# Kernel optimization log

Hardware: AMD Instinct MI355X
Metric: run time of the kernel (lower is better)

## Reference

```python
import jax, jax.numpy as jnp
import numpy as np

B, S, D, H = 2, 2048, 1024, 16
DK = D // H  # 64

def setup_inputs() -> dict:
    key = jax.random.key(0)
    ks = jax.random.split(key, 8)
    xavier = np.sqrt(6.0 / (D + D))  # xavier_uniform bound for square Linear
    def lin_w(k):
        return jax.random.uniform(k, (D, D), jnp.float32, -xavier, xavier)
    return {
        'Q': jax.random.normal(ks[0], (B, S, D), jnp.float32),
        'length': jax.random.randint(ks[1], (B,), 1, S + 1, jnp.int32),
        'Wq': lin_w(ks[2]), 'bq': jnp.zeros((D,), jnp.float32),
        'Wk': lin_w(ks[3]), 'bk': jnp.zeros((D,), jnp.float32),
        'Wv': lin_w(ks[4]), 'bv': jnp.zeros((D,), jnp.float32),
    }

def reference(Q, length, Wq, bq, Wk, bk, Wv, bv):
    # project and split heads: [B,S,D] -> [B,H,S,DK]
    def heads(x, W, b):
        y = jnp.einsum('bsd,de->bse', x, W) + b
        return y.reshape(B, S, H, DK).transpose(0, 2, 1, 3)
    q = heads(Q, Wq, bq)
    k = heads(Q, Wk, bk)
    v = heads(Q, Wv, bv)
    scores = jnp.einsum('bhqd,bhkd->bhqk', q, k) / np.sqrt(DK)
    scores = jnp.exp(scores)  # NOTE: raw exp, no max-subtraction (faithful)
    # multiplicative key mask: mask[b,k] = k < length[b], broadcast over q,h
    mask = (jnp.arange(S)[None, :] < length[:, None]).astype(scores.dtype)
    scores = scores * mask[:, None, None, :]
    attn = scores / (jnp.sum(scores, axis=-1, keepdims=True) + 1e-8)
    ctx = jnp.einsum('bhqk,bhkd->bhqd', attn, v)
    return ctx.transpose(0, 2, 1, 3).reshape(B, S, D)
```

## Files before the change

kernel.cpp:

```cpp
#include <hip/hip_runtime.h>
#include <hip/hip_bf16.h>

#define B_  2
#define S_  2048
#define D_  1024
#define H_  16
#define DK_ 64
#define M_  (B_ * S_)

typedef short short8 __attribute__((ext_vector_type(8)));
typedef float float4v __attribute__((ext_vector_type(4)));

#define QSCALE 0.18033688011112042f

static __device__ __forceinline__ ushort f32_to_bf16bits(float f) {
    union { __hip_bfloat16 h; ushort u; } cv;
    cv.h = __float2bfloat16(f);
    return cv.u;
}

static __device__ __forceinline__ void glds16(const ushort* g, ushort* l) {
    __builtin_amdgcn_global_load_lds(
        (const __attribute__((address_space(1))) unsigned int*)g,
        (__attribute__((address_space(3))) unsigned int*)l, 16, 0, 0);
}

__global__ __launch_bounds__(256) void prep(
    const float* __restrict__ X, const float* __restrict__ W0,
    const float* __restrict__ W1, const float* __restrict__ W2,
    ushort* __restrict__ Xb, ushort* __restrict__ Wt)
{
    const int z = blockIdx.z;
    const int t = threadIdx.x;

    if (z >= 3) {
        const int blk = (z - 3) * 256 + blockIdx.y * 16 + blockIdx.x;
        const int i = blk * 2048 + t * 8;
        float4v a = *(const float4v*)(X + i);
        float4v b = *(const float4v*)(X + i + 4);
        short8 o;
        o[0] = (short)f32_to_bf16bits(a[0]); o[1] = (short)f32_to_bf16bits(a[1]);
        o[2] = (short)f32_to_bf16bits(a[2]); o[3] = (short)f32_to_bf16bits(a[3]);
        o[4] = (short)f32_to_bf16bits(b[0]); o[5] = (short)f32_to_bf16bits(b[1]);
        o[6] = (short)f32_to_bf16bits(b[2]); o[7] = (short)f32_to_bf16bits(b[3]);
        *(short8*)(Xb + i) = o;
        return;
    }

    const float* W = (z == 0) ? W0 : ((z == 1) ? W1 : W2);
    ushort* out = Wt + (size_t)z * D_ * D_;

    __shared__ ushort tile[64 * 72];
    int n0 = blockIdx.x * 64, k0 = blockIdx.y * 64;
    int r = t >> 3, g = t & 7;

    #pragma unroll
    for (int p = 0; p < 2; ++p) {
        int rr = r + p * 32;
        const float* src = W + (size_t)(k0 + rr) * D_ + n0 + g * 8;
        float4v a = *(const float4v*)src;
        float4v b = *(const float4v*)(src + 4);
        short8 o;
        o[0] = (short)f32_to_bf16bits(a[0]); o[1] = (short)f32_to_bf16bits(a[1]);
        o[2] = (short)f32_to_bf16bits(a[2]); o[3] = (short)f32_to_bf16bits(a[3]);
        o[4] = (short)f32_to_bf16bits(b[0]); o[5] = (short)f32_to_bf16bits(b[1]);
        o[6] = (short)f32_to_bf16bits(b[2]); o[7] = (short)f32_to_bf16bits(b[3]);
        *(short8*)&tile[rr * 72 + g * 8] = o;
    }
    __syncthreads();
    #pragma unroll
    for (int p = 0; p < 2; ++p) {
        int rr = r + p * 32;
        short8 v;
        #pragma unroll
        for (int i = 0; i < 8; ++i)
            v[i] = (short)tile[(g * 8 + i) * 72 + rr];
        *(short8*)(out + (size_t)(n0 + rr) * D_ + k0 + g * 8) = v;
    }
}

__global__ __launch_bounds__(256, 2) void proj_gemm(
    const ushort* __restrict__ X,
    const ushort* __restrict__ Wt,
    const float* __restrict__ b0, const float* __restrict__ b1,
    const float* __restrict__ b2,
    const int* __restrict__ length,
    ushort* __restrict__ qkv)
{
    const int m0 = blockIdx.x * 64, n0 = blockIdx.y * 128;
    const int bidx = m0 >> 11;
    const int s0 = m0 & (S_ - 1);
    const bool kv = (s0 < length[bidx]);

    __shared__ __align__(16) ushort As[64 * 64];
    __shared__ __align__(16) ushort Bs[3][128 * 64];

    const int t = threadIdx.x;
    const int lane = t & 63, wid = t >> 6;
    const int quad = lane >> 4, l16 = lane & 15;
    const int wr = wid >> 1, wc = wid & 1;

    float4v accq[2][4] = {}, acck[2][4] = {}, accv[2][4] = {};

    for (int kt = 0; kt < 16; ++kt) {
        const int k0 = kt * 64;
        __syncthreads();
        #pragma unroll
        for (int j = 0; j < 2; ++j) {
            const int cid = wid * 128 + j * 64 + lane;
            const int row = cid >> 3;
            const int cl  = (cid & 7) ^ (row & 7);
            glds16(X + (size_t)(m0 + row) * D_ + k0 + cl * 8, &As[cid * 8]);
        }
        #pragma unroll
        for (int j = 0; j < 4; ++j) {
            const int cid = wid * 256 + j * 64 + lane;
            const int row = cid >> 3;
            const int cl  = (cid & 7) ^ (row & 7);
            const size_t off = (size_t)(n0 + row) * D_ + k0 + cl * 8;
            glds16(Wt + off, &Bs[0][cid * 8]);
            if (kv) {
                glds16(Wt + (size_t)D_ * D_ + off,     &Bs[1][cid * 8]);
                glds16(Wt + (size_t)2 * D_ * D_ + off, &Bs[2][cid * 8]);
            }
        }
        __syncthreads();

        #pragma unroll
        for (int ks = 0; ks < 2; ++ks) {
            short8 a[2];
            #pragma unroll
            for (int i = 0; i < 2; ++i) {
                const int r = wr * 32 + i * 16 + l16;
                const int ph = (ks * 4 + quad) ^ (r & 7);
                a[i] = *(short8*)&As[r * 64 + ph * 8];
            }
            short8 bq[4];
            #pragma unroll
            for (int j = 0; j < 4; ++j) {
                const int r = wc * 64 + j * 16 + l16;
                const int ph = (ks * 4 + quad) ^ (r & 7);
                bq[j] = *(short8*)&Bs[0][r * 64 + ph * 8];
            }
            #pragma unroll
            for (int i = 0; i < 2; ++i)
                #pragma unroll
                for (int j = 0; j < 4; ++j)
                    accq[i][j] = __builtin_amdgcn_mfma_f32_16x16x32_bf16(
                        a[i], bq[j], accq[i][j], 0, 0, 0);
            if (kv) {
                short8 bk[4], bv[4];
                #pragma unroll
                for (int j = 0; j < 4; ++j) {
                    const int r = wc * 64 + j * 16 + l16;
                    const int ph = (ks * 4 + quad) ^ (r & 7);
                    bk[j] = *(short8*)&Bs[1][r * 64 + ph * 8];
                    bv[j] = *(short8*)&Bs[2][r * 64 + ph * 8];
                }
                #pragma unroll
                for (int i = 0; i < 2; ++i)
                    #pragma unroll
                    for (int j = 0; j < 4; ++j) {
                        acck[i][j] = __builtin_amdgcn_mfma_f32_16x16x32_bf16(
                            a[i], bk[j], acck[i][j], 0, 0, 0);
                        accv[i][j] = __builtin_amdgcn_mfma_f32_16x16x32_bf16(
                            a[i], bv[j], accv[i][j], 0, 0, 0);
                    }
            }
        }
    }

    #pragma unroll
    for (int j = 0; j < 4; ++j) {
        const int col = n0 + wc * 64 + j * 16 + l16;
        const int h = col >> 6, dk = col & (DK_ - 1);
        const float bvq = b0[col], bvk = b1[col], bvv = b2[col];
        #pragma unroll
        for (int i = 0; i < 2; ++i) {
            #pragma unroll
            for (int rr = 0; rr < 4; ++rr) {
                const int row = m0 + wr * 32 + i * 16 + quad * 4 + rr;
                const int s = row & (S_ - 1);
                const size_t hdr = ((size_t)(bidx * H_ + h) * S_ + s) * DK_ + dk;
                qkv[hdr] = f32_to_bf16bits((accq[i][j][rr] + bvq) * QSCALE);
                if (kv) {
                    qkv[(size_t)M_ * D_ + hdr] =
                        f32_to_bf16bits(acck[i][j][rr] + bvk);
                    qkv[(size_t)2 * M_ * D_ +
                        ((size_t)(bidx * H_ + h) * DK_ + dk) * S_ + s] =
                        f32_to_bf16bits(accv[i][j][rr] + bvv);
                }
            }
        }
    }
}

__global__ __launch_bounds__(256, 3) void attention(
    const ushort* __restrict__ qkv, const int* __restrict__ length,
    float* __restrict__ out)
{
    const int bid  = blockIdx.x;
    const int work = (bid & 7) * 128 + (bid >> 3);
    const int q0 = (work & 31) * 64;
    const int bh = work >> 5;
    const int b  = bh & 1;
    const int h  = bh >> 1;

    int len = length[b];
    if (len > S_) len = S_;
    if (len < 1) len = 1;
    const int nkt = (len + 63) >> 6;

    const ushort* qb = qkv + ((size_t)(b * H_ + h) * S_ + q0) * DK_;
    const ushort* kb = qkv + (size_t)M_ * D_ + (size_t)(b * H_ + h) * S_ * DK_;
    const ushort* vb = qkv + (size_t)2 * M_ * D_ + (size_t)(b * H_ + h) * DK_ * S_;

    __shared__ __align__(16) ushort Ks[3][64 * 64];
    __shared__ __align__(16) ushort Vs[3][64 * 64];

    const int t = threadIdx.x, lane = t & 63, wid = t >> 6;
    const int quad = lane >> 4, l16 = lane & 15;

    const int klocal = ((l16 >> 2) << 3) + (l16 & 3);
    const int hk     = (l16 & 3) | (((l16 >> 2) & 1) << 2);

    short8 qfrag[2];
    {
        const ushort* qp = qb + (size_t)(wid * 16 + l16) * DK_;
        qfrag[0] = *(const short8*)(qp + quad * 8);
        qfrag[1] = *(const short8*)(qp + (4 + quad) * 8);
    }

    auto stageKV = [&](int buf, int tile) {
        #pragma unroll
        for (int j = 0; j < 2; ++j) {
            const int cid = wid * 128 + j * 64 + lane;
            const int row = cid >> 3;
            const int c   = cid & 7;
            const int hKr = (row & 3) | (((row >> 3) & 1) << 2);
            glds16(kb + (size_t)(tile * 64 + row) * DK_ + (c ^ hKr) * 8,
                   &Ks[buf][cid * 8]);
            glds16(vb + (size_t)row * S_ + tile * 64 + (c ^ (row & 7)) * 8,
                   &Vs[buf][cid * 8]);
        }
    };

    stageKV(0, 0);
    if (nkt > 1) stageKV(1, 1);

    short8 ones8;
    #pragma unroll
    for (int i = 0; i < 8; ++i) ones8[i] = (short)0x3F80;

    float4v cacc[4] = {};
    float4v racc = {};

    int cur = 0;
    for (int kt = 0; kt < nkt; ++kt) {
        if (kt == nkt - 1) {
            asm volatile("s_waitcnt vmcnt(0) lgkmcnt(0)" ::: "memory");
        } else {
            asm volatile("s_waitcnt vmcnt(4) lgkmcnt(0)" ::: "memory");
        }
        __builtin_amdgcn_sched_barrier(0);
        __builtin_amdgcn_s_barrier();
        __builtin_amdgcn_sched_barrier(0);

        if (kt + 2 < nkt) {
            int sb = cur + 2; if (sb >= 3) sb -= 3;
            stageKV(sb, kt + 2);
        }

        float4v sacc[4] = {};
        #pragma unroll
        for (int ks = 0; ks < 2; ++ks) {
            #pragma unroll
            for (int ct = 0; ct < 4; ++ct) {
                const int krow = ((ct >> 1) << 5) + ((ct & 1) << 2) + klocal;
                const int pha = (ks * 4 + quad) ^ hk;
                short8 ak = *(short8*)&Ks[cur][krow * 64 + pha * 8];
                sacc[ct] = __builtin_amdgcn_mfma_f32_16x16x32_bf16(
                    ak, qfrag[ks], sacc[ct], 0, 0, 0);
            }
        }

        const bool full = ((kt + 1) * 64 <= len);
        short8 ap[2];
        #pragma unroll
        for (int ks = 0; ks < 2; ++ks) {
            union { uint u[4]; short8 s; } cv;
            #pragma unroll
            for (int hh = 0; hh < 2; ++hh) {
                const int ct = 2 * ks + hh;
                float e0 = __builtin_amdgcn_exp2f(sacc[ct][0]);
                float e1 = __builtin_amdgcn_exp2f(sacc[ct][1]);
                float e2 = __builtin_amdgcn_exp2f(sacc[ct][2]);
                float e3 = __builtin_amdgcn_exp2f(sacc[ct][3]);
                if (!full) {
                    const int kb0 = kt * 64 + ks * 32 + quad * 8 + hh * 4;
                    e0 = (kb0 + 0 < len) ? e0 : 0.f;
                    e1 = (kb0 + 1 < len) ? e1 : 0.f;
                    e2 = (kb0 + 2 < len) ? e2 : 0.f;
                    e3 = (kb0 + 3 < len) ? e3 : 0.f;
                }
                cv.u[hh * 2 + 0] = (__float_as_uint(e0) >> 16) |
                                   (__float_as_uint(e1) & 0xFFFF0000u);
                cv.u[hh * 2 + 1] = (__float_as_uint(e2) >> 16) |
                                   (__float_as_uint(e3) & 0xFFFF0000u);
            }
            ap[ks] = cv.s;
        }

        #pragma unroll
        for (int ks = 0; ks < 2; ++ks) {
            #pragma unroll
            for (int ct = 0; ct < 4; ++ct) {
                const int vrow = ct * 16 + l16;
                const int phv = (ks * 4 + quad) ^ (vrow & 7);
                short8 vv = *(short8*)&Vs[cur][vrow * 64 + phv * 8];
                cacc[ct] = __builtin_amdgcn_mfma_f32_16x16x32_bf16(
                    ap[ks], vv, cacc[ct], 0, 0, 0);
            }
            racc = __builtin_amdgcn_mfma_f32_16x16x32_bf16(
                ap[ks], ones8, racc, 0, 0, 0);
        }

        cur = cur + 1; if (cur == 3) cur = 0;
    }

    #pragma unroll
    for (int rr = 0; rr < 4; ++rr) {
        const float inv = 1.0f / (racc[rr] + 1e-8f);
        const int q = q0 + wid * 16 + quad * 4 + rr;
        #pragma unroll
        for (int ct = 0; ct < 4; ++ct) {
            const int d = h * 64 + ct * 16 + l16;
            out[((size_t)b * S_ + q) * D_ + d] = cacc[ct][rr] * inv;
        }
    }
}

extern "C" void kernel_launch(void* const* d_in, const int* in_sizes, int n_in,
                              void* d_out, int out_size, void* d_ws, size_t ws_size,
                              hipStream_t stream)
{
    const float* Q   = (const float*)d_in[0];
    const int*   len = (const int*)d_in[1];
    const float* Wq  = (const float*)d_in[2];
    const float* bq  = (const float*)d_in[3];
    const float* Wk  = (const float*)d_in[4];
    const float* bk  = (const float*)d_in[5];
    const float* Wv  = (const float*)d_in[6];
    const float* bv  = (const float*)d_in[7];
    float* out = (float*)d_out;

    ushort* ws  = (ushort*)d_ws;
    ushort* Xb  = ws;
    ushort* Wt  = ws + (size_t)M_ * D_;
    ushort* qkv = Wt + (size_t)3 * D_ * D_;

    dim3 gPr(16, 16, 11);
    prep<<<gPr, 256, 0, stream>>>(Q, Wq, Wk, Wv, Xb, Wt);

    dim3 gP(M_ / 64, D_ / 128);
    proj_gemm<<<gP, 256, 0, stream>>>(Xb, Wt, bq, bk, bv, len, qkv);

    attention<<<dim3(S_ / 64 * H_ * B_), 256, 0, stream>>>(qkv, len, out);
}
```

Before: 152.3 us.

## Process 128 queries per attention block to reuse staged K/V tiles

Each attention workgroup now covers 128 query rows instead of 64, so every wave runs two 16-row query tiles against each K/V tile staged in LDS. This halves the number of workgroups and the total K/V global-to-LDS traffic, and reuses each LDS fragment read across two MFMA chains. The block-to-work mapping is rewritten to match, and launch bounds drop from 3 to 2 blocks per CU to allow the larger accumulator register footprint. In exchange there are fewer blocks (512) to cover the GPU and lower occupancy.

```diff
diff --git a/kernel.cpp b/kernel.cpp
--- a/kernel.cpp
+++ b/kernel.cpp
@@ -195,16 +195,16 @@
     }
 }
 
-__global__ __launch_bounds__(256, 3) void attention(
+__global__ __launch_bounds__(256, 2) void attention(
     const ushort* __restrict__ qkv, const int* __restrict__ length,
     float* __restrict__ out)
 {
     const int bid  = blockIdx.x;
-    const int work = (bid & 7) * 128 + (bid >> 3);
-    const int q0 = (work & 31) * 64;
-    const int bh = work >> 5;
-    const int b  = bh & 1;
-    const int h  = bh >> 1;
+    const int work = (bid & 7) * 64 + (bid >> 3);
+    const int q0   = (work & 15) * 128;
+    const int hlo  = (work >> 4) & 1;
+    const int b    = (work >> 5) & 1;
+    const int h    = ((work >> 6) << 1) | hlo;
 
     int len = length[b];
     if (len > S_) len = S_;
@@ -224,11 +224,12 @@
     const int klocal = ((l16 >> 2) << 3) + (l16 & 3);
     const int hk     = (l16 & 3) | (((l16 >> 2) & 1) << 2);
 
-    short8 qfrag[2];
-    {
-        const ushort* qp = qb + (size_t)(wid * 16 + l16) * DK_;
-        qfrag[0] = *(const short8*)(qp + quad * 8);
-        qfrag[1] = *(const short8*)(qp + (4 + quad) * 8);
+    short8 qfrag[2][2];
+    #pragma unroll
+    for (int qt = 0; qt < 2; ++qt) {
+        const ushort* qp = qb + (size_t)(wid * 32 + qt * 16 + l16) * DK_;
+        qfrag[qt][0] = *(const short8*)(qp + quad * 8);
+        qfrag[qt][1] = *(const short8*)(qp + (4 + quad) * 8);
     }
 
     auto stageKV = [&](int buf, int tile) {
@@ -252,8 +253,8 @@
     #pragma unroll
     for (int i = 0; i < 8; ++i) ones8[i] = (short)0x3F80;
 
-    float4v cacc[4] = {};
-    float4v racc = {};
+    float4v cacc[2][4] = {};
+    float4v racc[2] = {};
 
     int cur = 0;
     for (int kt = 0; kt < nkt; ++kt) {
@@ -271,7 +272,7 @@
             stageKV(sb, kt + 2);
         }
 
-        float4v sacc[4] = {};
+        float4v sacc[2][4] = {};
         #pragma unroll
         for (int ks = 0; ks < 2; ++ks) {
             #pragma unroll
@@ -279,36 +280,41 @@
                 const int krow = ((ct >> 1) << 5) + ((ct & 1) << 2) + klocal;
                 const int pha = (ks * 4 + quad) ^ hk;
                 short8 ak = *(short8*)&Ks[cur][krow * 64 + pha * 8];
-                sacc[ct] = __builtin_amdgcn_mfma_f32_16x16x32_bf16(
-                    ak, qfrag[ks], sacc[ct], 0, 0, 0);
+                sacc[0][ct] = __builtin_amdgcn_mfma_f32_16x16x32_bf16(
+                    ak, qfrag[0][ks], sacc[0][ct], 0, 0, 0);
+                sacc[1][ct] = __builtin_amdgcn_mfma_f32_16x16x32_bf16(
+                    ak, qfrag[1][ks], sacc[1][ct], 0, 0, 0);
             }
         }
 
         const bool full = ((kt + 1) * 64 <= len);
-        short8 ap[2];
-        #pragma unroll
-        for (int ks = 0; ks < 2; ++ks) {
-            union { uint u[4]; short8 s; } cv;
-            #pragma unroll
-            for (int hh = 0; hh < 2; ++hh) {
-                const int ct = 2 * ks + hh;
-                float e0 = __builtin_amdgcn_exp2f(sacc[ct][0]);
-                float e1 = __builtin_amdgcn_exp2f(sacc[ct][1]);
-                float e2 = __builtin_amdgcn_exp2f(sacc[ct][2]);
-                float e3 = __builtin_amdgcn_exp2f(sacc[ct][3]);
-                if (!full) {
-                    const int kb0 = kt * 64 + ks * 32 + quad * 8 + hh * 4;
-                    e0 = (kb0 + 0 < len) ? e0 : 0.f;
-                    e1 = (kb0 + 1 < len) ? e1 : 0.f;
-                    e2 = (kb0 + 2 < len) ? e2 : 0.f;
-                    e3 = (kb0 + 3 < len) ? e3 : 0.f;
+        short8 ap[2][2];
+        #pragma unroll
+        for (int qt = 0; qt < 2; ++qt) {
+            #pragma unroll
+            for (int ks = 0; ks < 2; ++ks) {
+                union { uint u[4]; short8 s; } cv;
+                #pragma unroll
+                for (int hh = 0; hh < 2; ++hh) {
+                    const int ct = 2 * ks + hh;
+                    float e0 = __builtin_amdgcn_exp2f(sacc[qt][ct][0]);
+                    float e1 = __builtin_amdgcn_exp2f(sacc[qt][ct][1]);
+                    float e2 = __builtin_amdgcn_exp2f(sacc[qt][ct][2]);
+                    float e3 = __builtin_amdgcn_exp2f(sacc[qt][ct][3]);
+                    if (!full) {
+                        const int kb0 = kt * 64 + ks * 32 + quad * 8 + hh * 4;
+                        e0 = (kb0 + 0 < len) ? e0 : 0.f;
+                        e1 = (kb0 + 1 < len) ? e1 : 0.f;
+                        e2 = (kb0 + 2 < len) ? e2 : 0.f;
+                        e3 = (kb0 + 3 < len) ? e3 : 0.f;
+                    }
+                    cv.u[hh * 2 + 0] = (__float_as_uint(e0) >> 16) |
+                                       (__float_as_uint(e1) & 0xFFFF0000u);
+                    cv.u[hh * 2 + 1] = (__float_as_uint(e2) >> 16) |
+                                       (__float_as_uint(e3) & 0xFFFF0000u);
                 }
-                cv.u[hh * 2 + 0] = (__float_as_uint(e0) >> 16) |
-                                   (__float_as_uint(e1) & 0xFFFF0000u);
-                cv.u[hh * 2 + 1] = (__float_as_uint(e2) >> 16) |
-                                   (__float_as_uint(e3) & 0xFFFF0000u);
-            }
-            ap[ks] = cv.s;
+                ap[qt][ks] = cv.s;
+            }
         }
 
         #pragma unroll
@@ -318,24 +324,31 @@
                 const int vrow = ct * 16 + l16;
                 const int phv = (ks * 4 + quad) ^ (vrow & 7);
                 short8 vv = *(short8*)&Vs[cur][vrow * 64 + phv * 8];
-                cacc[ct] = __builtin_amdgcn_mfma_f32_16x16x32_bf16(
-                    ap[ks], vv, cacc[ct], 0, 0, 0);
-            }
-            racc = __builtin_amdgcn_mfma_f32_16x16x32_bf16(
-                ap[ks], ones8, racc, 0, 0, 0);
+                cacc[0][ct] = __builtin_amdgcn_mfma_f32_16x16x32_bf16(
+                    ap[0][ks], vv, cacc[0][ct], 0, 0, 0);
+                cacc[1][ct] = __builtin_amdgcn_mfma_f32_16x16x32_bf16(
+                    ap[1][ks], vv, cacc[1][ct], 0, 0, 0);
+            }
+            racc[0] = __builtin_amdgcn_mfma_f32_16x16x32_bf16(
+                ap[0][ks], ones8, racc[0], 0, 0, 0);
+            racc[1] = __builtin_amdgcn_mfma_f32_16x16x32_bf16(
+                ap[1][ks], ones8, racc[1], 0, 0, 0);
         }
 
         cur = cur + 1; if (cur == 3) cur = 0;
     }
 
     #pragma unroll
-    for (int rr = 0; rr < 4; ++rr) {
-        const float inv = 1.0f / (racc[rr] + 1e-8f);
-        const int q = q0 + wid * 16 + quad * 4 + rr;
-        #pragma unroll
-        for (int ct = 0; ct < 4; ++ct) {
-            const int d = h * 64 + ct * 16 + l16;
-            out[((size_t)b * S_ + q) * D_ + d] = cacc[ct][rr] * inv;
+    for (int qt = 0; qt < 2; ++qt) {
+        #pragma unroll
+        for (int rr = 0; rr < 4; ++rr) {
+            const float inv = 1.0f / (racc[qt][rr] + 1e-8f);
+            const int q = q0 + wid * 32 + qt * 16 + quad * 4 + rr;
+            #pragma unroll
+            for (int ct = 0; ct < 4; ++ct) {
+                const int d = h * 64 + ct * 16 + l16;
+                out[((size_t)b * S_ + q) * D_ + d] = cacc[qt][ct][rr] * inv;
+            }
         }
     }
 }
@@ -365,5 +378,5 @@
     dim3 gP(M_ / 64, D_ / 128);
     proj_gemm<<<gP, 256, 0, stream>>>(Xb, Wt, bq, bk, bv, len, qkv);
 
-    attention<<<dim3(S_ / 64 * H_ * B_), 256, 0, stream>>>(qkv, len, out);
-}
+    attention<<<dim3(S_ / 128 * H_ * B_), 256, 0, stream>>>(qkv, len, out);
+}
```

Result: slower. 156.3 us (+2.6%).
